# Performance work log

Measured on AMD Instinct MI355X. Metric: run time of the kernel, lower is better.

Reference implementation:

```python
import jax, jax.numpy as jnp
from jax import lax
import numpy as np

WS = 32          # window size
NUM_AA = 21      # one-hot alphabet size (hardcoded in original forward)
L = 2048         # sequence length
WIDTH = 2048
IN_SIZE = WS * NUM_AA + WS  # 704


def setup_inputs() -> dict:
    key = jax.random.key(0)
    ks = jax.random.split(key, 8)
    x = jax.random.randint(ks[0], (L,), 0, NUM_AA, dtype=jnp.int32)
    gain = np.sqrt(2.0)  # relu gain, xavier_normal init
    def xavier(k, fan_out, fan_in):
        std = gain * np.sqrt(2.0 / (fan_in + fan_out))
        return jax.random.normal(k, (fan_out, fan_in), dtype=jnp.float32) * std
    inp = {"x": x}
    dims = [(WIDTH, IN_SIZE), (WIDTH, WIDTH), (WIDTH, WIDTH), (WIDTH, WIDTH), (WIDTH, WIDTH), (1, WIDTH)]
    for i, (fo, fi) in enumerate(dims):
        inp[f"W{i}"] = xavier(ks[i + 1], fo, fi)
        inp[f"b{i}"] = jnp.zeros((fo,), dtype=jnp.float32)
    return inp


def reference(x, W0, b0, W1, b1, W2, b2, W3, b3, W4, b4, W5, b5):
    Ws = (W0, W1, W2, W3, W4, W5)
    bs = (b0, b1, b2, b3, b4, b5)
    n = x.shape[0]
    # one-hot features; the sliding window of the last WS one-hots is
    onehot = jax.nn.one_hot(x, NUM_AA, dtype=jnp.float32)          # [n, 21]
    padded = jnp.concatenate([jnp.zeros((WS - 1, NUM_AA), jnp.float32), onehot], axis=0)
    idx = jnp.arange(n)[:, None] + jnp.arange(WS)[None, :]          # [n, WS]
    xfeat = padded[idx].reshape(n, WS * NUM_AA)                     # [n, 672]

    def step(y_window, xf):
        # y_window: last WS predictions (init zeros, matching original)
        h = jnp.concatenate([xf, y_window])                         # [704]
        for W, b in zip(Ws, bs):
            h = jax.nn.relu(W @ h + b)  # relu after EVERY layer incl. output
        y_window = jnp.concatenate([y_window[1:], h])               # h: [1]
        return y_window, h[0]

    _, ys = lax.scan(step, jnp.zeros((WS,), jnp.float32), xfeat)
    return ys  # [n] predictions, equivalent of torch.cat(y_pred[ws:])
```

## Files before the change

kernel.cpp:

```cpp
#include <hip/hip_runtime.h>
#include <stdint.h>


typedef uint32_t u32;
typedef _Float16 half_t;
typedef _Float16 half2_t __attribute__((ext_vector_type(2)));

#define L_SEQ 2048
#define WIDTH 2048
#define WS    32
#define NAA   21
#define INS   704

__device__ __forceinline__ float h2f(u32 b){
  union { unsigned short u; half_t h; } c; c.u = (unsigned short)(b & 0xffffu);
  return (float)c.h;
}
__device__ __forceinline__ u32 f2h(float f){
  union { unsigned short u; half_t h; } c; c.h = (half_t)f;
  return (u32)c.u;
}
__device__ __forceinline__ float fdot2f(u32 a, u32 b, float c){
#if __has_builtin(__builtin_amdgcn_fdot2)
  union { u32 u; half2_t v; } ca, cb; ca.u = a; cb.u = b;
  return __builtin_amdgcn_fdot2(ca.v, cb.v, c, false);
#else
  return c + h2f(a)*h2f(b) + h2f(a>>16)*h2f(b>>16);
#endif
}
__device__ __forceinline__ u32 aload(u32* p){
  return __hip_atomic_load(p, __ATOMIC_RELAXED, __HIP_MEMORY_SCOPE_AGENT);
}
__device__ __forceinline__ void astore(u32* p, u32 v){
  __hip_atomic_store(p, v, __ATOMIC_RELAXED, __HIP_MEMORY_SCOPE_AGENT);
}

__global__ void k_wt(const float* __restrict__ W0, float* __restrict__ W0T){
  int tid = blockIdx.x*256 + threadIdx.x;
  if (tid < INS*WIDTH){
    int c = tid >> 11, i = tid & 2047;
    W0T[(size_t)c*WIDTH + i] = W0[(size_t)i*INS + c];
  }
}

__global__ void k_wc(const float* __restrict__ A, const float* __restrict__ B,
                     const float* __restrict__ C, const float* __restrict__ D,
                     uint4* __restrict__ Wp){
  int b = blockIdx.x; int l = b >> 11; int r = b & 2047; int j = threadIdx.x;
  const float* S = (l==0)?A:(l==1)?B:(l==2)?C:D;
  const float* rowp = S + (size_t)r*WIDTH;
  u32 o[4];
  #pragma unroll
  for (int q=0;q<4;++q){
    float a = rowp[(size_t)(2*q+0)*256 + j];
    float c2= rowp[(size_t)(2*q+1)*256 + j];
    o[q] = f2h(a) | (f2h(c2) << 16);
  }
  Wp[(size_t)b*256 + j] = make_uint4(o[0],o[1],o[2],o[3]);
}

__global__ void k_c0(const int* __restrict__ x, const float* __restrict__ W0T,
                     const float* __restrict__ b0, uint4* __restrict__ c0p){
  int t = blockIdx.x, j = threadIdx.x;
  __shared__ int cidx[WS];
  if (j < WS){
    int s = t - (WS-1) + j;
    cidx[j] = (s >= 0) ? (NAA*j + x[s]) : -1;
  }
  __syncthreads();
  float acc[8];
  #pragma unroll
  for (int k=0;k<8;++k) acc[k] = b0[256*k + j];
  for (int m=0;m<WS;++m){
    int c = cidx[m];
    if (c >= 0){
      const float* col = W0T + (size_t)c*WIDTH;
      #pragma unroll
      for (int k=0;k<8;++k) acc[k] += col[256*k + j];
    }
  }
  u32 o[4];
  #pragma unroll
  for (int q=0;q<4;++q) o[q] = f2h(acc[2*q]) | (f2h(acc[2*q+1]) << 16);
  c0p[(size_t)t*256 + j] = make_uint4(o[0],o[1],o[2],o[3]);
}

__global__ void k_reset(u32* __restrict__ hb, u32* __restrict__ pb){
  int tid = blockIdx.x*256 + threadIdx.x;
  if (tid < 3*WIDTH) hb[tid] = 0xFFFFFFFFu;
  if (tid < 256)     pb[tid] = 0xFFFFFFFFu;
}

__global__ __launch_bounds__(256, 1) void k_main(
    const float* __restrict__ W0,
    const float* __restrict__ b1, const float* __restrict__ b2,
    const float* __restrict__ b3, const float* __restrict__ b4,
    const float* __restrict__ W5, const float* __restrict__ b5p,
    const uint4* __restrict__ Wp, const uint4* __restrict__ c0p,
    u32* __restrict__ hb, u32* __restrict__ pb, float* __restrict__ out)
{
  const int j  = threadIdx.x;
  const int X  = blockIdx.x;
  const int r8 = j & 7;
  const int row = 8*X + r8;

  __shared__ float red[4][8];
  __shared__ float redp[4];

  u32 w0y[8][16];
  float w31[8];
  #pragma unroll
  for (int k=0;k<8;++k){
    const float4* bp = (const float4*)(W0 + (size_t)(256*k + j)*INS + (INS - WS));
    float arr[32];
    #pragma unroll
    for (int q=0;q<8;++q){
      float4 v = bp[q];
      arr[4*q+0]=v.x; arr[4*q+1]=v.y; arr[4*q+2]=v.z; arr[4*q+3]=v.w;
    }
    #pragma unroll
    for (int p=0;p<16;++p) w0y[k][p] = f2h(arr[2*p]) | (f2h(arr[2*p+1]) << 16);
    w31[k] = arr[31];
  }
  const float w5v = W5[row];
  const float b5v = b5p[0];
  float bsc[4] = { b1[row], b2[row], b3[row], b4[row] };

  u32 yqp[16];
  #pragma unroll
  for (int p=0;p<16;++p) yqp[p] = 0u;
  float u_part[8];
  #pragma unroll
  for (int k=0;k<8;++k) u_part[k] = 0.f;

  uint4 wrow[8];
  u32 hh[4];
  const size_t LSTR = (size_t)WIDTH*256;

  auto dolayer = [&](){
    float accv[8];
    #pragma unroll
    for (int r=0;r<8;++r){
      float a = 0.f;
      a = fdot2f(wrow[r].x, hh[0], a);
      a = fdot2f(wrow[r].y, hh[1], a);
      a = fdot2f(wrow[r].z, hh[2], a);
      a = fdot2f(wrow[r].w, hh[3], a);
      #pragma unroll
      for (int d=1; d<64; d<<=1) a += __shfl_xor(a, d);
      accv[r] = a;
    }
    if ((j & 63) == 0){
      const int w = j >> 6;
      #pragma unroll
      for (int r=0;r<8;++r) red[w][r] = accv[r];
    }
    __syncthreads();
  };

  auto pollh = [&](int l, u32 tag){
    u32 v[8];
    for(;;){
      bool ok = true;
      #pragma unroll
      for (int k=0;k<8;++k){
        v[k] = aload(&hb[l*WIDTH + 256*k + j]);
        ok &= ((v[k] >> 16) == tag);
      }
      if (ok) break;
    }
    #pragma unroll
    for (int q=0;q<4;++q) hh[q] = (v[2*q] & 0xffffu) | (v[2*q+1] << 16);
  };

  #pragma unroll 1
  for (int t=0; t<L_SEQ; ++t){
    #pragma unroll
    for (int r=0;r<8;++r) wrow[r] = Wp[(size_t)(8*X + r)*256 + j];
    uint4 c0v = c0p[(size_t)t*256 + j];

    float yprev = 0.f;
    if (t > 0){
      u32 pv;
      do { pv = aload(&pb[j]); } while ((pv >> 16) != (u32)(t-1));
      float p = h2f(pv);
      #pragma unroll
      for (int d=1; d<64; d<<=1) p += __shfl_xor(p, d);
      if ((j & 63) == 0) redp[j >> 6] = p;
      __syncthreads();
      float y = fmaxf(redp[0]+redp[1]+redp[2]+redp[3] + b5v, 0.f);
      if (X == 0 && j == 0) out[t-1] = y;
      yprev = y;
      yqp[15] |= (f2h(y) << 16);
    }

    {
      u32 c0h[4] = { c0v.x, c0v.y, c0v.z, c0v.w };
      float h0v[8];
      #pragma unroll
      for (int k=0;k<8;++k){
        u32 cb = (k & 1) ? (c0h[k>>1] >> 16) : c0h[k>>1];
        h0v[k] = fmaxf(h2f(cb) + u_part[k] + w31[k]*yprev, 0.f);
      }
      #pragma unroll
      for (int q=0;q<4;++q) hh[q] = f2h(h0v[2*q]) | (f2h(h0v[2*q+1]) << 16);
    }

    dolayer();
    if (j < 8){
      float s = fmaxf(red[0][j]+red[1][j]+red[2][j]+red[3][j] + bsc[0], 0.f);
      astore(&hb[0*WIDTH + row], ((u32)t << 16) | f2h(s));
    }
    __syncthreads();
    #pragma unroll
    for (int r=0;r<8;++r) wrow[r] = Wp[LSTR + (size_t)(8*X + r)*256 + j];
    {
      #pragma unroll
      for (int p=0;p<15;++p) yqp[p] = (yqp[p] >> 16) | (yqp[p+1] << 16);
      yqp[15] = (yqp[15] >> 16);
      #pragma unroll
      for (int k=0;k<8;++k){
        float a = 0.f;
        #pragma unroll
        for (int p=0;p<16;++p) a = fdot2f(w0y[k][p], yqp[p], a);
        u_part[k] = a;
      }
    }
    pollh(0, (u32)t);

    dolayer();
    if (j < 8){
      float s = fmaxf(red[0][j]+red[1][j]+red[2][j]+red[3][j] + bsc[1], 0.f);
      astore(&hb[1*WIDTH + row], ((u32)t << 16) | f2h(s));
    }
    __syncthreads();
    #pragma unroll
    for (int r=0;r<8;++r) wrow[r] = Wp[2*LSTR + (size_t)(8*X + r)*256 + j];
    pollh(1, (u32)t);

    dolayer();
    if (j < 8){
      float s = fmaxf(red[0][j]+red[1][j]+red[2][j]+red[3][j] + bsc[2], 0.f);
      astore(&hb[2*WIDTH + row], ((u32)t << 16) | f2h(s));
    }
    __syncthreads();
    #pragma unroll
    for (int r=0;r<8;++r) wrow[r] = Wp[3*LSTR + (size_t)(8*X + r)*256 + j];
    pollh(2, (u32)t);

    dolayer();
    if (j < 8){
      float s = fmaxf(red[0][j]+red[1][j]+red[2][j]+red[3][j] + bsc[3], 0.f);
      float pp = s * w5v;
      pp += __shfl_xor(pp, 1);
      pp += __shfl_xor(pp, 2);
      pp += __shfl_xor(pp, 4);
      if (j == 0) astore(&pb[X], ((u32)t << 16) | f2h(pp));
    }
  }

  if (X == 0){
    u32 pv;
    do { pv = aload(&pb[j]); } while ((pv >> 16) != (u32)(L_SEQ-1));
    float p = h2f(pv);
    #pragma unroll
    for (int d=1; d<64; d<<=1) p += __shfl_xor(p, d);
    if ((j & 63) == 0) redp[j >> 6] = p;
    __syncthreads();
    if (j == 0) out[L_SEQ-1] = fmaxf(redp[0]+redp[1]+redp[2]+redp[3] + b5v, 0.f);
  }
}

extern "C" void kernel_launch(void* const* d_in, const int* in_sizes, int n_in,
                              void* d_out, int out_size, void* d_ws, size_t ws_size,
                              hipStream_t stream) {
  (void)in_sizes; (void)n_in; (void)out_size; (void)ws_size;
  const int*   x  = (const int*)  d_in[0];
  const float* W0 = (const float*)d_in[1];
  const float* b0 = (const float*)d_in[2];
  const float* W1 = (const float*)d_in[3];
  const float* b1 = (const float*)d_in[4];
  const float* W2 = (const float*)d_in[5];
  const float* b2 = (const float*)d_in[6];
  const float* W3 = (const float*)d_in[7];
  const float* b3 = (const float*)d_in[8];
  const float* W4 = (const float*)d_in[9];
  const float* b4 = (const float*)d_in[10];
  const float* W5 = (const float*)d_in[11];
  const float* b5 = (const float*)d_in[12];
  float* out = (float*)d_out;
  char*  ws  = (char*)d_ws;

  constexpr size_t OFF_WP  = 0;
  constexpr size_t OFF_C0  = 33554432;
  constexpr size_t OFF_W0T = 41943040;
  constexpr size_t OFF_HB  = 47710208;
  constexpr size_t OFF_PB  = 47734784;

  uint4* Wp  = (uint4*)(ws + OFF_WP);
  uint4* c0p = (uint4*)(ws + OFF_C0);
  float* W0T = (float*)(ws + OFF_W0T);
  u32*   hb  = (u32*)  (ws + OFF_HB);
  u32*   pb  = (u32*)  (ws + OFF_PB);

  k_wt   <<<5632, 256, 0, stream>>>(W0, W0T);
  k_wc   <<<8192, 256, 0, stream>>>(W1, W2, W3, W4, Wp);
  k_c0   <<<2048, 256, 0, stream>>>(x, W0T, b0, c0p);
  k_reset<<<24,   256, 0, stream>>>(hb, pb);
  k_main <<<256,  256, 0, stream>>>(W0, b1, b2, b3, b4, W5, b5,
                                    Wp, c0p, hb, pb, out);
}
```

Measured before the change: 22.36 ms.

## Halve persistent blocks, pack hidden-state exchange into 64-bit tagged records

The persistent recurrent kernel now runs on 128 blocks with 16 rows each instead of 256 blocks with 8 rows, which halves the number of participants in each cross-block flag exchange. Hidden activations are exchanged as 64-bit records holding four fp16 values plus a tag, so each thread polls four words instead of eight. Features are now laid out contiguously per thread, so the preprocessing kernels can use vectorized float4 loads. The butterfly reduction is also restructured to pair rows across lanes, and the output partial sums are read as packed pairs by a single wavefront. In exchange, each block does twice the dot-product work per layer and holds more weight registers, which raises per-step compute latency.

```diff
diff --git a/kernel.cpp b/kernel.cpp
--- a/kernel.cpp
+++ b/kernel.cpp
@@ -3,6 +3,7 @@
 
 
 typedef uint32_t u32;
+typedef unsigned long long ull;
 typedef _Float16 half_t;
 typedef _Float16 half2_t __attribute__((ext_vector_type(2)));
 
@@ -11,6 +12,9 @@
 #define WS    32
 #define NAA   21
 #define INS   704
+#define NB    128
+#define RPB   16
+#define RECS  1024
 
 __device__ __forceinline__ float h2f(u32 b){
   union { unsigned short u; half_t h; } c; c.u = (unsigned short)(b & 0xffffu);
@@ -34,6 +38,12 @@
 __device__ __forceinline__ void astore(u32* p, u32 v){
   __hip_atomic_store(p, v, __ATOMIC_RELAXED, __HIP_MEMORY_SCOPE_AGENT);
 }
+__device__ __forceinline__ ull aload64(ull* p){
+  return __hip_atomic_load(p, __ATOMIC_RELAXED, __HIP_MEMORY_SCOPE_AGENT);
+}
+__device__ __forceinline__ void astore64(ull* p, ull v){
+  __hip_atomic_store(p, v, __ATOMIC_RELAXED, __HIP_MEMORY_SCOPE_AGENT);
+}
 
 __global__ void k_wt(const float* __restrict__ W0, float* __restrict__ W0T){
   int tid = blockIdx.x*256 + threadIdx.x;
@@ -48,15 +58,13 @@
                      uint4* __restrict__ Wp){
   int b = blockIdx.x; int l = b >> 11; int r = b & 2047; int j = threadIdx.x;
   const float* S = (l==0)?A:(l==1)?B:(l==2)?C:D;
-  const float* rowp = S + (size_t)r*WIDTH;
-  u32 o[4];
-  #pragma unroll
-  for (int q=0;q<4;++q){
-    float a = rowp[(size_t)(2*q+0)*256 + j];
-    float c2= rowp[(size_t)(2*q+1)*256 + j];
-    o[q] = f2h(a) | (f2h(c2) << 16);
-  }
-  Wp[(size_t)b*256 + j] = make_uint4(o[0],o[1],o[2],o[3]);
+  const float4* rowp = (const float4*)(S + (size_t)r*WIDTH + 8*j);
+  float4 v0 = rowp[0], v1 = rowp[1];
+  u32 o0 = f2h(v0.x) | (f2h(v0.y) << 16);
+  u32 o1 = f2h(v0.z) | (f2h(v0.w) << 16);
+  u32 o2 = f2h(v1.x) | (f2h(v1.y) << 16);
+  u32 o3 = f2h(v1.z) | (f2h(v1.w) << 16);
+  Wp[(size_t)b*256 + j] = make_uint4(o0,o1,o2,o3);
 }
 
 __global__ void k_c0(const int* __restrict__ x, const float* __restrict__ W0T,
@@ -69,14 +77,17 @@
   }
   __syncthreads();
   float acc[8];
-  #pragma unroll
-  for (int k=0;k<8;++k) acc[k] = b0[256*k + j];
+  const float4* bp = (const float4*)(b0 + 8*j);
+  float4 b00 = bp[0], b01 = bp[1];
+  acc[0]=b00.x; acc[1]=b00.y; acc[2]=b00.z; acc[3]=b00.w;
+  acc[4]=b01.x; acc[5]=b01.y; acc[6]=b01.z; acc[7]=b01.w;
   for (int m=0;m<WS;++m){
     int c = cidx[m];
     if (c >= 0){
-      const float* col = W0T + (size_t)c*WIDTH;
-      #pragma unroll
-      for (int k=0;k<8;++k) acc[k] += col[256*k + j];
+      const float4* col = (const float4*)(W0T + (size_t)c*WIDTH + 8*j);
+      float4 u0 = col[0], u1 = col[1];
+      acc[0]+=u0.x; acc[1]+=u0.y; acc[2]+=u0.z; acc[3]+=u0.w;
+      acc[4]+=u1.x; acc[5]+=u1.y; acc[6]+=u1.z; acc[7]+=u1.w;
     }
   }
   u32 o[4];
@@ -88,7 +99,7 @@
 __global__ void k_reset(u32* __restrict__ hb, u32* __restrict__ pb){
   int tid = blockIdx.x*256 + threadIdx.x;
   if (tid < 3*WIDTH) hb[tid] = 0xFFFFFFFFu;
-  if (tid < 256)     pb[tid] = 0xFFFFFFFFu;
+  if (tid < NB)      pb[tid] = 0xFFFFFFFFu;
 }
 
 __global__ __launch_bounds__(256, 1) void k_main(
@@ -97,21 +108,20 @@
     const float* __restrict__ b3, const float* __restrict__ b4,
     const float* __restrict__ W5, const float* __restrict__ b5p,
     const uint4* __restrict__ Wp, const uint4* __restrict__ c0p,
-    u32* __restrict__ hb, u32* __restrict__ pb, float* __restrict__ out)
+    ull* hbq, ull* pbq, u32* pb, float* __restrict__ out)
 {
-  const int j  = threadIdx.x;
-  const int X  = blockIdx.x;
-  const int r8 = j & 7;
-  const int row = 8*X + r8;
-
-  __shared__ float red[4][8];
-  __shared__ float redp[4];
+  const int j = threadIdx.x;
+  const int X = blockIdx.x;
+  const int row16 = RPB*X + (j & 15);
+
+  __shared__ float red[4][RPB];
+  __shared__ float ylds;
 
   u32 w0y[8][16];
   float w31[8];
   #pragma unroll
-  for (int k=0;k<8;++k){
-    const float4* bp = (const float4*)(W0 + (size_t)(256*k + j)*INS + (INS - WS));
+  for (int e=0;e<8;++e){
+    const float4* bp = (const float4*)(W0 + (size_t)(8*j + e)*INS + (INS - WS));
     float arr[32];
     #pragma unroll
     for (int q=0;q<8;++q){
@@ -119,155 +129,174 @@
       arr[4*q+0]=v.x; arr[4*q+1]=v.y; arr[4*q+2]=v.z; arr[4*q+3]=v.w;
     }
     #pragma unroll
-    for (int p=0;p<16;++p) w0y[k][p] = f2h(arr[2*p]) | (f2h(arr[2*p+1]) << 16);
-    w31[k] = arr[31];
-  }
-  const float w5v = W5[row];
+    for (int p=0;p<16;++p) w0y[e][p] = f2h(arr[2*p]) | (f2h(arr[2*p+1]) << 16);
+    w31[e] = arr[31];
+  }
+  const float w5v = W5[row16];
   const float b5v = b5p[0];
-  float bsc[4] = { b1[row], b2[row], b3[row], b4[row] };
+  float bsc[4] = { b1[row16], b2[row16], b3[row16], b4[row16] };
 
   u32 yqp[16];
   #pragma unroll
   for (int p=0;p<16;++p) yqp[p] = 0u;
   float u_part[8];
   #pragma unroll
-  for (int k=0;k<8;++k) u_part[k] = 0.f;
-
-  uint4 wrow[8];
+  for (int e=0;e<8;++e) u_part[e] = 0.f;
+
+  uint4 wrow[RPB];
   u32 hh[4];
-  const size_t LSTR = (size_t)WIDTH*256;
-
-  auto dolayer = [&](){
-    float accv[8];
-    #pragma unroll
-    for (int r=0;r<8;++r){
+  const int w = j >> 6;
+
+  auto prefetch = [&](int lw){
+    #pragma unroll
+    for (int r=0;r<RPB;++r)
+      wrow[r] = Wp[((size_t)lw*2048 + RPB*X + r)*256 + j];
+  };
+
+  auto doreduce = [&](){
+    float accv[RPB];
+    #pragma unroll
+    for (int r=0;r<RPB;++r){
       float a = 0.f;
       a = fdot2f(wrow[r].x, hh[0], a);
       a = fdot2f(wrow[r].y, hh[1], a);
       a = fdot2f(wrow[r].z, hh[2], a);
       a = fdot2f(wrow[r].w, hh[3], a);
-      #pragma unroll
-      for (int d=1; d<64; d<<=1) a += __shfl_xor(a, d);
       accv[r] = a;
     }
-    if ((j & 63) == 0){
-      const int w = j >> 6;
-      #pragma unroll
-      for (int r=0;r<8;++r) red[w][r] = accv[r];
+    #pragma unroll
+    for (int r=0;r<RPB;r+=2){
+      float a = accv[r]   + __shfl_xor(accv[r],   1);
+      float b = accv[r+1] + __shfl_xor(accv[r+1], 1);
+      float m = (j & 1) ? b : a;
+      m += __shfl_xor(m, 2);
+      m += __shfl_xor(m, 4);
+      m += __shfl_xor(m, 8);
+      m += __shfl_xor(m, 16);
+      m += __shfl_xor(m, 32);
+      if ((j & 63) < 2) red[w][r + (j & 1)] = m;
     }
     __syncthreads();
   };
 
+  auto emit_h = [&](int l, u32 tag, float bias){
+    float s = 0.f;
+    if (j < 16) s = fmaxf(red[0][j]+red[1][j]+red[2][j]+red[3][j] + bias, 0.f);
+    if (j < 64){
+      u32 hs = f2h(s);
+      u32 lo = __shfl(hs, 2*j);
+      u32 hi = __shfl(hs, 2*j + 1);
+      if (j < 8)
+        astore64(hbq + (size_t)l*RECS + 8*X + j,
+                 ((ull)tag << 32) | (ull)(lo | (hi << 16)));
+    }
+  };
+
   auto pollh = [&](int l, u32 tag){
-    u32 v[8];
+    ull* base = hbq + (size_t)l*RECS + 4*j;
+    ull r0,r1,r2,r3;
     for(;;){
-      bool ok = true;
-      #pragma unroll
-      for (int k=0;k<8;++k){
-        v[k] = aload(&hb[l*WIDTH + 256*k + j]);
-        ok &= ((v[k] >> 16) == tag);
-      }
-      if (ok) break;
-    }
-    #pragma unroll
-    for (int q=0;q<4;++q) hh[q] = (v[2*q] & 0xffffu) | (v[2*q+1] << 16);
+      r0 = aload64(base+0); r1 = aload64(base+1);
+      r2 = aload64(base+2); r3 = aload64(base+3);
+      if (((u32)(r0>>32)==tag) & ((u32)(r1>>32)==tag) &
+          ((u32)(r2>>32)==tag) & ((u32)(r3>>32)==tag)) break;
+    }
+    hh[0]=(u32)r0; hh[1]=(u32)r1; hh[2]=(u32)r2; hh[3]=(u32)r3;
   };
 
   #pragma unroll 1
   for (int t=0; t<L_SEQ; ++t){
-    #pragma unroll
-    for (int r=0;r<8;++r) wrow[r] = Wp[(size_t)(8*X + r)*256 + j];
+    prefetch(0);
     uint4 c0v = c0p[(size_t)t*256 + j];
 
-    float yprev = 0.f;
     if (t > 0){
-      u32 pv;
-      do { pv = aload(&pb[j]); } while ((pv >> 16) != (u32)(t-1));
-      float p = h2f(pv);
-      #pragma unroll
-      for (int d=1; d<64; d<<=1) p += __shfl_xor(p, d);
-      if ((j & 63) == 0) redp[j >> 6] = p;
-      __syncthreads();
-      float y = fmaxf(redp[0]+redp[1]+redp[2]+redp[3] + b5v, 0.f);
-      if (X == 0 && j == 0) out[t-1] = y;
-      yprev = y;
-      yqp[15] |= (f2h(y) << 16);
-    }
+      if (j < 64){
+        u32 lo, hi; ull v;
+        const u32 tprev = (u32)(t-1);
+        for(;;){
+          v = aload64(pbq + j);
+          lo = (u32)v; hi = (u32)(v >> 32);
+          if (((lo>>16)==tprev) & ((hi>>16)==tprev)) break;
+        }
+        float p = h2f(lo) + h2f(hi);
+        #pragma unroll
+        for (int d=1; d<64; d<<=1) p += __shfl_xor(p, d);
+        if (j == 0){
+          float y = fmaxf(p + b5v, 0.f);
+          ylds = y;
+          if (X == 0) out[t-1] = y;
+        }
+      }
+    } else {
+      if (j == 0) ylds = 0.f;
+    }
+    __syncthreads();
+    float yprev = ylds;
+    if (t > 0) yqp[15] |= (f2h(yprev) << 16);
 
     {
       u32 c0h[4] = { c0v.x, c0v.y, c0v.z, c0v.w };
       float h0v[8];
       #pragma unroll
-      for (int k=0;k<8;++k){
-        u32 cb = (k & 1) ? (c0h[k>>1] >> 16) : c0h[k>>1];
-        h0v[k] = fmaxf(h2f(cb) + u_part[k] + w31[k]*yprev, 0.f);
+      for (int e=0;e<8;++e){
+        u32 cb = (e & 1) ? (c0h[e>>1] >> 16) : c0h[e>>1];
+        h0v[e] = fmaxf(h2f(cb) + u_part[e] + w31[e]*yprev, 0.f);
       }
       #pragma unroll
       for (int q=0;q<4;++q) hh[q] = f2h(h0v[2*q]) | (f2h(h0v[2*q+1]) << 16);
     }
 
-    dolayer();
-    if (j < 8){
-      float s = fmaxf(red[0][j]+red[1][j]+red[2][j]+red[3][j] + bsc[0], 0.f);
-      astore(&hb[0*WIDTH + row], ((u32)t << 16) | f2h(s));
-    }
-    __syncthreads();
-    #pragma unroll
-    for (int r=0;r<8;++r) wrow[r] = Wp[LSTR + (size_t)(8*X + r)*256 + j];
+    doreduce();
+    emit_h(0, (u32)t, bsc[0]);
+    prefetch(1);
     {
       #pragma unroll
       for (int p=0;p<15;++p) yqp[p] = (yqp[p] >> 16) | (yqp[p+1] << 16);
       yqp[15] = (yqp[15] >> 16);
       #pragma unroll
-      for (int k=0;k<8;++k){
+      for (int e=0;e<8;++e){
         float a = 0.f;
         #pragma unroll
-        for (int p=0;p<16;++p) a = fdot2f(w0y[k][p], yqp[p], a);
-        u_part[k] = a;
+        for (int p=0;p<16;++p) a = fdot2f(w0y[e][p], yqp[p], a);
+        u_part[e] = a;
       }
     }
     pollh(0, (u32)t);
 
-    dolayer();
-    if (j < 8){
-      float s = fmaxf(red[0][j]+red[1][j]+red[2][j]+red[3][j] + bsc[1], 0.f);
-      astore(&hb[1*WIDTH + row], ((u32)t << 16) | f2h(s));
-    }
-    __syncthreads();
-    #pragma unroll
-    for (int r=0;r<8;++r) wrow[r] = Wp[2*LSTR + (size_t)(8*X + r)*256 + j];
+    doreduce();
+    emit_h(1, (u32)t, bsc[1]);
+    prefetch(2);
     pollh(1, (u32)t);
 
-    dolayer();
-    if (j < 8){
-      float s = fmaxf(red[0][j]+red[1][j]+red[2][j]+red[3][j] + bsc[2], 0.f);
-      astore(&hb[2*WIDTH + row], ((u32)t << 16) | f2h(s));
-    }
-    __syncthreads();
-    #pragma unroll
-    for (int r=0;r<8;++r) wrow[r] = Wp[3*LSTR + (size_t)(8*X + r)*256 + j];
+    doreduce();
+    emit_h(2, (u32)t, bsc[2]);
+    prefetch(3);
     pollh(2, (u32)t);
 
-    dolayer();
-    if (j < 8){
+    doreduce();
+    if (j < 16){
       float s = fmaxf(red[0][j]+red[1][j]+red[2][j]+red[3][j] + bsc[3], 0.f);
       float pp = s * w5v;
       pp += __shfl_xor(pp, 1);
       pp += __shfl_xor(pp, 2);
       pp += __shfl_xor(pp, 4);
+      pp += __shfl_xor(pp, 8);
       if (j == 0) astore(&pb[X], ((u32)t << 16) | f2h(pp));
     }
   }
 
-  if (X == 0){
-    u32 pv;
-    do { pv = aload(&pb[j]); } while ((pv >> 16) != (u32)(L_SEQ-1));
-    float p = h2f(pv);
+  if (X == 0 && j < 64){
+    u32 lo, hi; ull v;
+    const u32 tl = (u32)(L_SEQ-1);
+    for(;;){
+      v = aload64(pbq + j);
+      lo = (u32)v; hi = (u32)(v >> 32);
+      if (((lo>>16)==tl) & ((hi>>16)==tl)) break;
+    }
+    float p = h2f(lo) + h2f(hi);
     #pragma unroll
     for (int d=1; d<64; d<<=1) p += __shfl_xor(p, d);
-    if ((j & 63) == 0) redp[j >> 6] = p;
-    __syncthreads();
-    if (j == 0) out[L_SEQ-1] = fmaxf(redp[0]+redp[1]+redp[2]+redp[3] + b5v, 0.f);
+    if (j == 0) out[L_SEQ-1] = fmaxf(p + b5v, 0.f);
   }
 }
 
@@ -301,12 +330,14 @@
   uint4* c0p = (uint4*)(ws + OFF_C0);
   float* W0T = (float*)(ws + OFF_W0T);
   u32*   hb  = (u32*)  (ws + OFF_HB);
+  ull*   hbq = (ull*)  (ws + OFF_HB);
   u32*   pb  = (u32*)  (ws + OFF_PB);
+  ull*   pbq = (ull*)  (ws + OFF_PB);
 
   k_wt   <<<5632, 256, 0, stream>>>(W0, W0T);
   k_wc   <<<8192, 256, 0, stream>>>(W1, W2, W3, W4, Wp);
   k_c0   <<<2048, 256, 0, stream>>>(x, W0T, b0, c0p);
   k_reset<<<24,   256, 0, stream>>>(hb, pb);
-  k_main <<<256,  256, 0, stream>>>(W0, b1, b2, b3, b4, W5, b5,
-                                    Wp, c0p, hb, pb, out);
-}
+  k_main <<<NB,   256, 0, stream>>>(W0, b1, b2, b3, b4, W5, b5,
+                                    Wp, c0p, hbq, pbq, pb, out);
+}
```

After: 31.45 ms. +40.7%, slower.

## Keep layer weights in registers and pack hidden-state flags into 64-bit records

Applied to the files above, without the earlier changes.

All four hidden layers' fp16 weight slices are now loaded into registers once, instead of being re-fetched from global memory every timestep. Hidden activations are exchanged as 64-bit records holding a tag and four fp16 values, so each poll needs four loads per thread instead of eight. The per-layer reduction pairs rows to halve the shuffle count, and the LDS buffers are double-buffered so one __syncthreads per layer can go. Column ordering is changed to a contiguous float2 layout throughout, and polling is software-pipelined. The cost is much higher register pressure and a more intricate packing scheme.

```diff
diff --git a/kernel.cpp b/kernel.cpp
--- a/kernel.cpp
+++ b/kernel.cpp
@@ -3,6 +3,7 @@
 
 
 typedef uint32_t u32;
+typedef unsigned long long ull;
 typedef _Float16 half_t;
 typedef _Float16 half2_t __attribute__((ext_vector_type(2)));
 
@@ -11,6 +12,8 @@
 #define WS    32
 #define NAA   21
 #define INS   704
+#define NB    256
+#define RECS  1024
 
 __device__ __forceinline__ float h2f(u32 b){
   union { unsigned short u; half_t h; } c; c.u = (unsigned short)(b & 0xffffu);
@@ -34,6 +37,12 @@
 __device__ __forceinline__ void astore(u32* p, u32 v){
   __hip_atomic_store(p, v, __ATOMIC_RELAXED, __HIP_MEMORY_SCOPE_AGENT);
 }
+__device__ __forceinline__ ull aload64(ull* p){
+  return __hip_atomic_load(p, __ATOMIC_RELAXED, __HIP_MEMORY_SCOPE_AGENT);
+}
+__device__ __forceinline__ void astore64(ull* p, ull v){
+  __hip_atomic_store(p, v, __ATOMIC_RELAXED, __HIP_MEMORY_SCOPE_AGENT);
+}
 
 __global__ void k_wt(const float* __restrict__ W0, float* __restrict__ W0T){
   int tid = blockIdx.x*256 + threadIdx.x;
@@ -48,13 +57,12 @@
                      uint4* __restrict__ Wp){
   int b = blockIdx.x; int l = b >> 11; int r = b & 2047; int j = threadIdx.x;
   const float* S = (l==0)?A:(l==1)?B:(l==2)?C:D;
-  const float* rowp = S + (size_t)r*WIDTH;
+  const float2* p2 = (const float2*)(S + (size_t)r*WIDTH);
   u32 o[4];
   #pragma unroll
-  for (int q=0;q<4;++q){
-    float a = rowp[(size_t)(2*q+0)*256 + j];
-    float c2= rowp[(size_t)(2*q+1)*256 + j];
-    o[q] = f2h(a) | (f2h(c2) << 16);
+  for (int k=0;k<4;++k){
+    float2 v = p2[256*k + j];
+    o[k] = f2h(v.x) | (f2h(v.y) << 16);
   }
   Wp[(size_t)b*256 + j] = make_uint4(o[0],o[1],o[2],o[3]);
 }
@@ -68,27 +76,28 @@
     cidx[j] = (s >= 0) ? (NAA*j + x[s]) : -1;
   }
   __syncthreads();
-  float acc[8];
-  #pragma unroll
-  for (int k=0;k<8;++k) acc[k] = b0[256*k + j];
+  float ax[4], ay[4];
+  const float2* b2p = (const float2*)b0;
+  #pragma unroll
+  for (int k=0;k<4;++k){ float2 v = b2p[256*k + j]; ax[k]=v.x; ay[k]=v.y; }
   for (int m=0;m<WS;++m){
     int c = cidx[m];
     if (c >= 0){
-      const float* col = W0T + (size_t)c*WIDTH;
-      #pragma unroll
-      for (int k=0;k<8;++k) acc[k] += col[256*k + j];
+      const float2* w2 = (const float2*)(W0T + (size_t)c*WIDTH);
+      #pragma unroll
+      for (int k=0;k<4;++k){ float2 v = w2[256*k + j]; ax[k]+=v.x; ay[k]+=v.y; }
     }
   }
   u32 o[4];
   #pragma unroll
-  for (int q=0;q<4;++q) o[q] = f2h(acc[2*q]) | (f2h(acc[2*q+1]) << 16);
+  for (int k=0;k<4;++k) o[k] = f2h(ax[k]) | (f2h(ay[k]) << 16);
   c0p[(size_t)t*256 + j] = make_uint4(o[0],o[1],o[2],o[3]);
 }
 
 __global__ void k_reset(u32* __restrict__ hb, u32* __restrict__ pb){
   int tid = blockIdx.x*256 + threadIdx.x;
   if (tid < 3*WIDTH) hb[tid] = 0xFFFFFFFFu;
-  if (tid < 256)     pb[tid] = 0xFFFFFFFFu;
+  if (tid < NB)      pb[tid] = 0xFFFFFFFFu;
 }
 
 __global__ __launch_bounds__(256, 1) void k_main(
@@ -97,31 +106,42 @@
     const float* __restrict__ b3, const float* __restrict__ b4,
     const float* __restrict__ W5, const float* __restrict__ b5p,
     const uint4* __restrict__ Wp, const uint4* __restrict__ c0p,
-    u32* __restrict__ hb, u32* __restrict__ pb, float* __restrict__ out)
+    ull* hbq, u32* pb, float* __restrict__ out)
 {
   const int j  = threadIdx.x;
   const int X  = blockIdx.x;
   const int r8 = j & 7;
   const int row = 8*X + r8;
 
-  __shared__ float red[4][8];
+  __shared__ float red[2][4][8];
   __shared__ float redp[4];
+
+  uint4 wreg[4][8];
+  #pragma unroll
+  for (int l=0;l<4;++l)
+    #pragma unroll
+    for (int r=0;r<8;++r)
+      wreg[l][r] = Wp[((size_t)l*2048 + 8*X + r)*256 + j];
 
   u32 w0y[8][16];
   float w31[8];
   #pragma unroll
-  for (int k=0;k<8;++k){
-    const float4* bp = (const float4*)(W0 + (size_t)(256*k + j)*INS + (INS - WS));
-    float arr[32];
-    #pragma unroll
-    for (int q=0;q<8;++q){
-      float4 v = bp[q];
-      arr[4*q+0]=v.x; arr[4*q+1]=v.y; arr[4*q+2]=v.z; arr[4*q+3]=v.w;
-    }
-    #pragma unroll
-    for (int p=0;p<16;++p) w0y[k][p] = f2h(arr[2*p]) | (f2h(arr[2*p+1]) << 16);
-    w31[k] = arr[31];
-  }
+  for (int k=0;k<4;++k)
+    #pragma unroll
+    for (int s=0;s<2;++s){
+      int e = 2*k+s;
+      int rr = 512*k + 2*j + s;
+      const float4* bp = (const float4*)(W0 + (size_t)rr*INS + (INS - WS));
+      float arr[32];
+      #pragma unroll
+      for (int q=0;q<8;++q){
+        float4 v = bp[q];
+        arr[4*q+0]=v.x; arr[4*q+1]=v.y; arr[4*q+2]=v.z; arr[4*q+3]=v.w;
+      }
+      #pragma unroll
+      for (int p=0;p<16;++p) w0y[e][p] = f2h(arr[2*p]) | (f2h(arr[2*p+1]) << 16);
+      w31[e] = arr[31];
+    }
   const float w5v = W5[row];
   const float b5v = b5p[0];
   float bsc[4] = { b1[row], b2[row], b3[row], b4[row] };
@@ -131,62 +151,86 @@
   for (int p=0;p<16;++p) yqp[p] = 0u;
   float u_part[8];
   #pragma unroll
-  for (int k=0;k<8;++k) u_part[k] = 0.f;
-
-  uint4 wrow[8];
+  for (int e=0;e<8;++e) u_part[e] = 0.f;
+
   u32 hh[4];
-  const size_t LSTR = (size_t)WIDTH*256;
-
-  auto dolayer = [&](){
+  const int w = j >> 6;
+
+  auto doreduce = [&](const uint4 (&wr)[8], int buf){
     float accv[8];
     #pragma unroll
     for (int r=0;r<8;++r){
       float a = 0.f;
-      a = fdot2f(wrow[r].x, hh[0], a);
-      a = fdot2f(wrow[r].y, hh[1], a);
-      a = fdot2f(wrow[r].z, hh[2], a);
-      a = fdot2f(wrow[r].w, hh[3], a);
-      #pragma unroll
-      for (int d=1; d<64; d<<=1) a += __shfl_xor(a, d);
+      a = fdot2f(wr[r].x, hh[0], a);
+      a = fdot2f(wr[r].y, hh[1], a);
+      a = fdot2f(wr[r].z, hh[2], a);
+      a = fdot2f(wr[r].w, hh[3], a);
       accv[r] = a;
     }
-    if ((j & 63) == 0){
-      const int w = j >> 6;
-      #pragma unroll
-      for (int r=0;r<8;++r) red[w][r] = accv[r];
+    #pragma unroll
+    for (int r=0;r<8;r+=2){
+      float a = accv[r]   + __shfl_xor(accv[r],   1);
+      float b = accv[r+1] + __shfl_xor(accv[r+1], 1);
+      float m = (j & 1) ? b : a;
+      m += __shfl_xor(m, 2);
+      m += __shfl_xor(m, 4);
+      m += __shfl_xor(m, 8);
+      m += __shfl_xor(m, 16);
+      m += __shfl_xor(m, 32);
+      if ((j & 63) < 2) red[buf][w][r + (j & 1)] = m;
     }
     __syncthreads();
   };
 
+  auto emit_h = [&](int l, u32 tag, float bias, int buf){
+    float s = 0.f;
+    if (j < 8)
+      s = fmaxf(red[buf][0][j]+red[buf][1][j]+red[buf][2][j]+red[buf][3][j] + bias, 0.f);
+    if (j < 64){
+      u32 hs = f2h(s);
+      u32 lo = __shfl(hs, 2*(j & 3));
+      u32 hi = __shfl(hs, 2*(j & 3) + 1);
+      if (j < 4)
+        astore64(hbq + (size_t)l*RECS + (X>>6)*256 + 4*(X&63) + j,
+                 ((ull)tag << 32) | (ull)(lo | (hi << 16)));
+    }
+  };
+
   auto pollh = [&](int l, u32 tag){
-    u32 v[8];
+    ull* base = hbq + (size_t)l*RECS;
+    ull A0,A1,A2,A3,B0,B1,B2,B3;
+    A0=aload64(base+     j); A1=aload64(base+ 256+j);
+    A2=aload64(base+ 512+j); A3=aload64(base+ 768+j);
+    B0=aload64(base+     j); B1=aload64(base+ 256+j);
+    B2=aload64(base+ 512+j); B3=aload64(base+ 768+j);
     for(;;){
-      bool ok = true;
-      #pragma unroll
-      for (int k=0;k<8;++k){
-        v[k] = aload(&hb[l*WIDTH + 256*k + j]);
-        ok &= ((v[k] >> 16) == tag);
-      }
-      if (ok) break;
-    }
-    #pragma unroll
-    for (int q=0;q<4;++q) hh[q] = (v[2*q] & 0xffffu) | (v[2*q+1] << 16);
+      if (((u32)(A0>>32)==tag) & ((u32)(A1>>32)==tag) &
+          ((u32)(A2>>32)==tag) & ((u32)(A3>>32)==tag)) break;
+      A0=B0; A1=B1; A2=B2; A3=B3;
+      B0=aload64(base+     j); B1=aload64(base+ 256+j);
+      B2=aload64(base+ 512+j); B3=aload64(base+ 768+j);
+    }
+    hh[0]=(u32)A0; hh[1]=(u32)A1; hh[2]=(u32)A2; hh[3]=(u32)A3;
   };
 
   #pragma unroll 1
   for (int t=0; t<L_SEQ; ++t){
-    #pragma unroll
-    for (int r=0;r<8;++r) wrow[r] = Wp[(size_t)(8*X + r)*256 + j];
     uint4 c0v = c0p[(size_t)t*256 + j];
 
     float yprev = 0.f;
     if (t > 0){
-      u32 pv;
-      do { pv = aload(&pb[j]); } while ((pv >> 16) != (u32)(t-1));
-      float p = h2f(pv);
+      const u32 tprev = (u32)(t-1);
+      u32 A = aload(&pb[j]);
+      u32 B = aload(&pb[j]);
+      for(;;){
+        if ((A >> 16) == tprev) break;
+        A = B;
+        B = aload(&pb[j]);
+      }
+      float p = h2f(A);
       #pragma unroll
       for (int d=1; d<64; d<<=1) p += __shfl_xor(p, d);
-      if ((j & 63) == 0) redp[j >> 6] = p;
+      if ((j & 63) == 0) redp[w] = p;
       __syncthreads();
       float y = fmaxf(redp[0]+redp[1]+redp[2]+redp[3] + b5v, 0.f);
       if (X == 0 && j == 0) out[t-1] = y;
@@ -196,76 +240,64 @@
 
     {
       u32 c0h[4] = { c0v.x, c0v.y, c0v.z, c0v.w };
-      float h0v[8];
-      #pragma unroll
-      for (int k=0;k<8;++k){
-        u32 cb = (k & 1) ? (c0h[k>>1] >> 16) : c0h[k>>1];
-        h0v[k] = fmaxf(h2f(cb) + u_part[k] + w31[k]*yprev, 0.f);
-      }
-      #pragma unroll
-      for (int q=0;q<4;++q) hh[q] = f2h(h0v[2*q]) | (f2h(h0v[2*q+1]) << 16);
-    }
-
-    dolayer();
-    if (j < 8){
-      float s = fmaxf(red[0][j]+red[1][j]+red[2][j]+red[3][j] + bsc[0], 0.f);
-      astore(&hb[0*WIDTH + row], ((u32)t << 16) | f2h(s));
-    }
-    __syncthreads();
-    #pragma unroll
-    for (int r=0;r<8;++r) wrow[r] = Wp[LSTR + (size_t)(8*X + r)*256 + j];
+      #pragma unroll
+      for (int k=0;k<4;++k){
+        float h0a = fmaxf(h2f(c0h[k])       + u_part[2*k]   + w31[2*k]*yprev,   0.f);
+        float h0b = fmaxf(h2f(c0h[k] >> 16) + u_part[2*k+1] + w31[2*k+1]*yprev, 0.f);
+        hh[k] = f2h(h0a) | (f2h(h0b) << 16);
+      }
+    }
+
+    doreduce(wreg[0], 0);
+    emit_h(0, (u32)t, bsc[0], 0);
     {
       #pragma unroll
       for (int p=0;p<15;++p) yqp[p] = (yqp[p] >> 16) | (yqp[p+1] << 16);
       yqp[15] = (yqp[15] >> 16);
       #pragma unroll
-      for (int k=0;k<8;++k){
+      for (int e=0;e<8;++e){
         float a = 0.f;
         #pragma unroll
-        for (int p=0;p<16;++p) a = fdot2f(w0y[k][p], yqp[p], a);
-        u_part[k] = a;
+        for (int p=0;p<16;++p) a = fdot2f(w0y[e][p], yqp[p], a);
+        u_part[e] = a;
       }
     }
     pollh(0, (u32)t);
 
-    dolayer();
-    if (j < 8){
-      float s = fmaxf(red[0][j]+red[1][j]+red[2][j]+red[3][j] + bsc[1], 0.f);
-      astore(&hb[1*WIDTH + row], ((u32)t << 16) | f2h(s));
-    }
-    __syncthreads();
-    #pragma unroll
-    for (int r=0;r<8;++r) wrow[r] = Wp[2*LSTR + (size_t)(8*X + r)*256 + j];
+    doreduce(wreg[1], 1);
+    emit_h(1, (u32)t, bsc[1], 1);
     pollh(1, (u32)t);
 
-    dolayer();
-    if (j < 8){
-      float s = fmaxf(red[0][j]+red[1][j]+red[2][j]+red[3][j] + bsc[2], 0.f);
-      astore(&hb[2*WIDTH + row], ((u32)t << 16) | f2h(s));
-    }
-    __syncthreads();
-    #pragma unroll
-    for (int r=0;r<8;++r) wrow[r] = Wp[3*LSTR + (size_t)(8*X + r)*256 + j];
+    doreduce(wreg[2], 0);
+    emit_h(2, (u32)t, bsc[2], 0);
     pollh(2, (u32)t);
 
-    dolayer();
-    if (j < 8){
-      float s = fmaxf(red[0][j]+red[1][j]+red[2][j]+red[3][j] + bsc[3], 0.f);
-      float pp = s * w5v;
-      pp += __shfl_xor(pp, 1);
-      pp += __shfl_xor(pp, 2);
-      pp += __shfl_xor(pp, 4);
-      if (j == 0) astore(&pb[X], ((u32)t << 16) | f2h(pp));
+    doreduce(wreg[3], 1);
+    {
+      float s = 0.f;
+      if (j < 8)
+        s = fmaxf(red[1][0][j]+red[1][1][j]+red[1][2][j]+red[1][3][j] + bsc[3], 0.f);
+      if (j < 64){
+        float pp = s * w5v;
+        pp += __shfl_xor(pp, 1);
+        pp += __shfl_xor(pp, 2);
+        pp += __shfl_xor(pp, 4);
+        if (j == 0) astore(&pb[X], ((u32)t << 16) | f2h(pp));
+      }
     }
   }
 
   if (X == 0){
-    u32 pv;
-    do { pv = aload(&pb[j]); } while ((pv >> 16) != (u32)(L_SEQ-1));
-    float p = h2f(pv);
+    const u32 tl = (u32)(L_SEQ-1);
+    u32 A = aload(&pb[j]);
+    for(;;){
+      if ((A >> 16) == tl) break;
+      A = aload(&pb[j]);
+    }
+    float p = h2f(A);
     #pragma unroll
     for (int d=1; d<64; d<<=1) p += __shfl_xor(p, d);
-    if ((j & 63) == 0) redp[j >> 6] = p;
+    if ((j & 63) == 0) redp[w] = p;
     __syncthreads();
     if (j == 0) out[L_SEQ-1] = fmaxf(redp[0]+redp[1]+redp[2]+redp[3] + b5v, 0.f);
   }
@@ -301,12 +333,13 @@
   uint4* c0p = (uint4*)(ws + OFF_C0);
   float* W0T = (float*)(ws + OFF_W0T);
   u32*   hb  = (u32*)  (ws + OFF_HB);
+  ull*   hbq = (ull*)  (ws + OFF_HB);
   u32*   pb  = (u32*)  (ws + OFF_PB);
 
   k_wt   <<<5632, 256, 0, stream>>>(W0, W0T);
   k_wc   <<<8192, 256, 0, stream>>>(W1, W2, W3, W4, Wp);
   k_c0   <<<2048, 256, 0, stream>>>(x, W0T, b0, c0p);
   k_reset<<<24,   256, 0, stream>>>(hb, pb);
-  k_main <<<256,  256, 0, stream>>>(W0, b1, b2, b3, b4, W5, b5,
-                                    Wp, c0p, hb, pb, out);
-}
+  k_main <<<NB,   256, 0, stream>>>(W0, b1, b2, b3, b4, W5, b5,
+                                    Wp, c0p, hbq, pb, out);
+}
```

Result: slower. 29.72 ms (+32.9%).

## Pipeline layers across block groups with register-resident weights

Applied to the files above, without the earlier changes.

The persistent kernel is split into four groups of 64 blocks, one per hidden layer. Each block keeps its 32 rows of fp16 weights in registers for the whole sequence instead of reloading 8 rows per layer per step, and each group polls only the previous layer's output buffer. The output layer's dot product moves into group 0, which reads layer-4 activations directly, and the y-window weights for W0 are stored in a workspace buffer instead of registers. Sleep-based backoff is added to the polling loops. This removes per-step weight reloads and lets different layers overlap, at the cost of higher register pressure, a multi-stage shuffle reduction, and added latency from the sleep calls.

```diff
diff --git a/kernel.cpp b/kernel.cpp
--- a/kernel.cpp
+++ b/kernel.cpp
@@ -11,6 +11,11 @@
 #define WS    32
 #define NAA   21
 #define INS   704
+#define NB    256
+#define GSZ   64
+#define SLP_FAIL 2
+#define SLP_IDLE 20
+#define N_IDLE   3
 
 __device__ __forceinline__ float h2f(u32 b){
   union { unsigned short u; half_t h; } c; c.u = (unsigned short)(b & 0xffffu);
@@ -48,14 +53,11 @@
                      uint4* __restrict__ Wp){
   int b = blockIdx.x; int l = b >> 11; int r = b & 2047; int j = threadIdx.x;
   const float* S = (l==0)?A:(l==1)?B:(l==2)?C:D;
-  const float* rowp = S + (size_t)r*WIDTH;
+  const float* row = S + (size_t)r*WIDTH;
   u32 o[4];
   #pragma unroll
-  for (int q=0;q<4;++q){
-    float a = rowp[(size_t)(2*q+0)*256 + j];
-    float c2= rowp[(size_t)(2*q+1)*256 + j];
-    o[q] = f2h(a) | (f2h(c2) << 16);
-  }
+  for (int q=0;q<4;++q)
+    o[q] = f2h(row[256*(2*q)+j]) | (f2h(row[256*(2*q+1)+j]) << 16);
   Wp[(size_t)b*256 + j] = make_uint4(o[0],o[1],o[2],o[3]);
 }
 
@@ -85,10 +87,17 @@
   c0p[(size_t)t*256 + j] = make_uint4(o[0],o[1],o[2],o[3]);
 }
 
-__global__ void k_reset(u32* __restrict__ hb, u32* __restrict__ pb){
+__global__ void k_wy(const float* __restrict__ W0, u32* __restrict__ wyb){
+  int b = blockIdx.x; int k = b >> 4, p = b & 15; int j = threadIdx.x;
+  int col = 256*k + j;
+  float a = W0[(size_t)col*INS + (INS-WS) + 2*p];
+  float c = W0[(size_t)col*INS + (INS-WS) + 2*p + 1];
+  wyb[(size_t)b*256 + j] = f2h(a) | (f2h(c) << 16);
+}
+
+__global__ void k_reset(u32* __restrict__ hb){
   int tid = blockIdx.x*256 + threadIdx.x;
-  if (tid < 3*WIDTH) hb[tid] = 0xFFFFFFFFu;
-  if (tid < 256)     pb[tid] = 0xFFFFFFFFu;
+  if (tid < 4*WIDTH) hb[tid] = 0xFFFFFFFFu;
 }
 
 __global__ __launch_bounds__(256, 1) void k_main(
@@ -97,177 +106,201 @@
     const float* __restrict__ b3, const float* __restrict__ b4,
     const float* __restrict__ W5, const float* __restrict__ b5p,
     const uint4* __restrict__ Wp, const uint4* __restrict__ c0p,
-    u32* __restrict__ hb, u32* __restrict__ pb, float* __restrict__ out)
+    const u32* __restrict__ wyb,
+    u32* hb, float* __restrict__ out)
 {
   const int j  = threadIdx.x;
   const int X  = blockIdx.x;
-  const int r8 = j & 7;
-  const int row = 8*X + r8;
-
-  __shared__ float red[4][8];
+  const int g  = X >> 6;
+  const int Xl = X & 63;
+  const int lw = j & 63;
+  const int w  = j >> 6;
+
+  __shared__ float red[4][32];
   __shared__ float redp[4];
 
-  u32 w0y[8][16];
-  float w31[8];
+  uint4 wreg[32];
   #pragma unroll
-  for (int k=0;k<8;++k){
-    const float4* bp = (const float4*)(W0 + (size_t)(256*k + j)*INS + (INS - WS));
-    float arr[32];
-    #pragma unroll
-    for (int q=0;q<8;++q){
-      float4 v = bp[q];
-      arr[4*q+0]=v.x; arr[4*q+1]=v.y; arr[4*q+2]=v.z; arr[4*q+3]=v.w;
-    }
-    #pragma unroll
-    for (int p=0;p<16;++p) w0y[k][p] = f2h(arr[2*p]) | (f2h(arr[2*p+1]) << 16);
-    w31[k] = arr[31];
-  }
-  const float w5v = W5[row];
-  const float b5v = b5p[0];
-  float bsc[4] = { b1[row], b2[row], b3[row], b4[row] };
-
-  u32 yqp[16];
-  #pragma unroll
-  for (int p=0;p<16;++p) yqp[p] = 0u;
-  float u_part[8];
-  #pragma unroll
-  for (int k=0;k<8;++k) u_part[k] = 0.f;
-
-  uint4 wrow[8];
+  for (int r=0;r<32;++r)
+    wreg[r] = Wp[((size_t)g*2048 + 32*Xl + r)*256 + j];
+
+  const float* bp = (g==0)?b1:(g==1)?b2:(g==2)?b3:b4;
+  float bv = 0.f;
+  if (j < 32) bv = bp[32*Xl + j];
+
   u32 hh[4];
-  const size_t LSTR = (size_t)WIDTH*256;
-
-  auto dolayer = [&](){
-    float accv[8];
-    #pragma unroll
-    for (int r=0;r<8;++r){
+
+  auto doreduce_emit = [&](u32 tag){
+    float c32[32];
+    #pragma unroll
+    for (int r=0;r<32;++r){
       float a = 0.f;
-      a = fdot2f(wrow[r].x, hh[0], a);
-      a = fdot2f(wrow[r].y, hh[1], a);
-      a = fdot2f(wrow[r].z, hh[2], a);
-      a = fdot2f(wrow[r].w, hh[3], a);
-      #pragma unroll
-      for (int d=1; d<64; d<<=1) a += __shfl_xor(a, d);
-      accv[r] = a;
-    }
-    if ((j & 63) == 0){
-      const int w = j >> 6;
-      #pragma unroll
-      for (int r=0;r<8;++r) red[w][r] = accv[r];
+      a = fdot2f(wreg[r].x, hh[0], a);
+      a = fdot2f(wreg[r].y, hh[1], a);
+      a = fdot2f(wreg[r].z, hh[2], a);
+      a = fdot2f(wreg[r].w, hh[3], a);
+      c32[r] = a;
+    }
+    float c16[16];
+    #pragma unroll
+    for (int i=0;i<16;++i){
+      float v = c32[2*i]   + __shfl_xor(c32[2*i],   1);
+      float u = c32[2*i+1] + __shfl_xor(c32[2*i+1], 1);
+      c16[i] = (lw & 1) ? u : v;
+    }
+    float c8[8];
+    #pragma unroll
+    for (int i=0;i<8;++i){
+      float v = c16[2*i]   + __shfl_xor(c16[2*i],   2);
+      float u = c16[2*i+1] + __shfl_xor(c16[2*i+1], 2);
+      c8[i] = (lw & 2) ? u : v;
+    }
+    float c4[4];
+    #pragma unroll
+    for (int i=0;i<4;++i){
+      float v = c8[2*i]   + __shfl_xor(c8[2*i],   4);
+      float u = c8[2*i+1] + __shfl_xor(c8[2*i+1], 4);
+      c4[i] = (lw & 4) ? u : v;
+    }
+    float c2[2];
+    #pragma unroll
+    for (int i=0;i<2;++i){
+      float v = c4[2*i]   + __shfl_xor(c4[2*i],   8);
+      float u = c4[2*i+1] + __shfl_xor(c4[2*i+1], 8);
+      c2[i] = (lw & 8) ? u : v;
+    }
+    float v1 = c2[0] + __shfl_xor(c2[0], 16);
+    float u1 = c2[1] + __shfl_xor(c2[1], 16);
+    float c1 = (lw & 16) ? u1 : v1;
+    float tot = c1 + __shfl_xor(c1, 32);
+    if (lw < 32) red[w][lw] = tot;
+    __syncthreads();
+    if (j < 32){
+      float s = fmaxf(red[0][j]+red[1][j]+red[2][j]+red[3][j] + bv, 0.f);
+      astore(&hb[(size_t)g*WIDTH + 32*Xl + j], (tag << 16) | f2h(s));
     }
     __syncthreads();
   };
 
-  auto pollh = [&](int l, u32 tag){
-    u32 v[8];
+  auto pollh = [&](int gin, u32 tag){
+    u32 rec[8];
+    u32* base = hb + (size_t)gin*WIDTH;
     for(;;){
+      #pragma unroll
+      for (int k=0;k<8;++k) rec[k] = aload(base + 256*k + j);
       bool ok = true;
       #pragma unroll
-      for (int k=0;k<8;++k){
-        v[k] = aload(&hb[l*WIDTH + 256*k + j]);
-        ok &= ((v[k] >> 16) == tag);
+      for (int k=0;k<8;++k) ok &= ((rec[k] >> 16) == tag);
+      if (ok) break;
+      __builtin_amdgcn_s_sleep(SLP_FAIL);
+    }
+    #pragma unroll
+    for (int q=0;q<4;++q) hh[q] = (rec[2*q] & 0xffffu) | (rec[2*q+1] << 16);
+  };
+
+  for (int i=0;i<g;++i) __builtin_amdgcn_s_sleep(SLP_IDLE);
+
+  if (g > 0){
+    const int gin = g - 1;
+    #pragma unroll 1
+    for (int t=0; t<L_SEQ; ++t){
+      pollh(gin, (u32)t);
+      doreduce_emit((u32)t);
+      for (int i=0;i<N_IDLE;++i) __builtin_amdgcn_s_sleep(SLP_IDLE);
+    }
+  } else {
+    float w5f[8], w31v[8];
+    #pragma unroll
+    for (int k=0;k<8;++k){
+      w5f[k]  = W5[256*k + j];
+      w31v[k] = W0[(size_t)(256*k + j)*INS + (INS-1)];
+    }
+    const float b5v = b5p[0];
+    u32 yqp[16];
+    #pragma unroll
+    for (int p=0;p<16;++p) yqp[p] = 0u;
+    float u_part[8];
+    #pragma unroll
+    for (int k=0;k<8;++k) u_part[k] = 0.f;
+
+    #pragma unroll 1
+    for (int t=0; t<L_SEQ; ++t){
+      float y = 0.f;
+      if (t > 0){
+        u32 rec[8];
+        u32* base = hb + (size_t)3*WIDTH;
+        const u32 tag = (u32)(t-1);
+        for(;;){
+          #pragma unroll
+          for (int k=0;k<8;++k) rec[k] = aload(base + 256*k + j);
+          bool ok = true;
+          #pragma unroll
+          for (int k=0;k<8;++k) ok &= ((rec[k] >> 16) == tag);
+          if (ok) break;
+          __builtin_amdgcn_s_sleep(SLP_FAIL);
+        }
+        float yp = 0.f;
+        #pragma unroll
+        for (int k=0;k<8;++k) yp += w5f[k] * h2f(rec[k]);
+        #pragma unroll
+        for (int d=1; d<64; d<<=1) yp += __shfl_xor(yp, d);
+        if (lw == 0) redp[w] = yp;
+        __syncthreads();
+        y = fmaxf(redp[0]+redp[1]+redp[2]+redp[3] + b5v, 0.f);
+        if (X == 0 && j == 0) out[t-1] = y;
+        yqp[15] |= (f2h(y) << 16);
       }
-      if (ok) break;
-    }
-    #pragma unroll
-    for (int q=0;q<4;++q) hh[q] = (v[2*q] & 0xffffu) | (v[2*q+1] << 16);
-  };
-
-  #pragma unroll 1
-  for (int t=0; t<L_SEQ; ++t){
-    #pragma unroll
-    for (int r=0;r<8;++r) wrow[r] = Wp[(size_t)(8*X + r)*256 + j];
-    uint4 c0v = c0p[(size_t)t*256 + j];
-
-    float yprev = 0.f;
-    if (t > 0){
-      u32 pv;
-      do { pv = aload(&pb[j]); } while ((pv >> 16) != (u32)(t-1));
-      float p = h2f(pv);
-      #pragma unroll
-      for (int d=1; d<64; d<<=1) p += __shfl_xor(p, d);
-      if ((j & 63) == 0) redp[j >> 6] = p;
+      uint4 c0v = c0p[(size_t)t*256 + j];
+      {
+        u32 c0h[4] = { c0v.x, c0v.y, c0v.z, c0v.w };
+        float h0v[8];
+        #pragma unroll
+        for (int q=0;q<4;++q){
+          h0v[2*q]   = fmaxf(h2f(c0h[q])       + u_part[2*q]   + w31v[2*q]*y,   0.f);
+          h0v[2*q+1] = fmaxf(h2f(c0h[q] >> 16) + u_part[2*q+1] + w31v[2*q+1]*y, 0.f);
+        }
+        #pragma unroll
+        for (int q=0;q<4;++q) hh[q] = f2h(h0v[2*q]) | (f2h(h0v[2*q+1]) << 16);
+      }
+      doreduce_emit((u32)t);
+      {
+        #pragma unroll
+        for (int p=0;p<15;++p) yqp[p] = (yqp[p] >> 16) | (yqp[p+1] << 16);
+        yqp[15] = (yqp[15] >> 16);
+        #pragma unroll
+        for (int k=0;k<8;++k){
+          float a = 0.f;
+          #pragma unroll
+          for (int p=0;p<16;++p)
+            a = fdot2f(wyb[(size_t)(16*k+p)*256 + j], yqp[p], a);
+          u_part[k] = a;
+        }
+      }
+      for (int i=0;i<N_IDLE;++i) __builtin_amdgcn_s_sleep(SLP_IDLE);
+    }
+
+    if (X == 0){
+      u32 rec[8];
+      u32* base = hb + (size_t)3*WIDTH;
+      const u32 tag = (u32)(L_SEQ-1);
+      for(;;){
+        #pragma unroll
+        for (int k=0;k<8;++k) rec[k] = aload(base + 256*k + j);
+        bool ok = true;
+        #pragma unroll
+        for (int k=0;k<8;++k) ok &= ((rec[k] >> 16) == tag);
+        if (ok) break;
+        __builtin_amdgcn_s_sleep(SLP_FAIL);
+      }
+      float yp = 0.f;
+      #pragma unroll
+      for (int k=0;k<8;++k) yp += w5f[k] * h2f(rec[k]);
+      #pragma unroll
+      for (int d=1; d<64; d<<=1) yp += __shfl_xor(yp, d);
+      if (lw == 0) redp[w] = yp;
       __syncthreads();
-      float y = fmaxf(redp[0]+redp[1]+redp[2]+redp[3] + b5v, 0.f);
-      if (X == 0 && j == 0) out[t-1] = y;
-      yprev = y;
-      yqp[15] |= (f2h(y) << 16);
-    }
-
-    {
-      u32 c0h[4] = { c0v.x, c0v.y, c0v.z, c0v.w };
-      float h0v[8];
-      #pragma unroll
-      for (int k=0;k<8;++k){
-        u32 cb = (k & 1) ? (c0h[k>>1] >> 16) : c0h[k>>1];
-        h0v[k] = fmaxf(h2f(cb) + u_part[k] + w31[k]*yprev, 0.f);
-      }
-      #pragma unroll
-      for (int q=0;q<4;++q) hh[q] = f2h(h0v[2*q]) | (f2h(h0v[2*q+1]) << 16);
-    }
-
-    dolayer();
-    if (j < 8){
-      float s = fmaxf(red[0][j]+red[1][j]+red[2][j]+red[3][j] + bsc[0], 0.f);
-      astore(&hb[0*WIDTH + row], ((u32)t << 16) | f2h(s));
-    }
-    __syncthreads();
-    #pragma unroll
-    for (int r=0;r<8;++r) wrow[r] = Wp[LSTR + (size_t)(8*X + r)*256 + j];
-    {
-      #pragma unroll
-      for (int p=0;p<15;++p) yqp[p] = (yqp[p] >> 16) | (yqp[p+1] << 16);
-      yqp[15] = (yqp[15] >> 16);
-      #pragma unroll
-      for (int k=0;k<8;++k){
-        float a = 0.f;
-        #pragma unroll
-        for (int p=0;p<16;++p) a = fdot2f(w0y[k][p], yqp[p], a);
-        u_part[k] = a;
-      }
-    }
-    pollh(0, (u32)t);
-
-    dolayer();
-    if (j < 8){
-      float s = fmaxf(red[0][j]+red[1][j]+red[2][j]+red[3][j] + bsc[1], 0.f);
-      astore(&hb[1*WIDTH + row], ((u32)t << 16) | f2h(s));
-    }
-    __syncthreads();
-    #pragma unroll
-    for (int r=0;r<8;++r) wrow[r] = Wp[2*LSTR + (size_t)(8*X + r)*256 + j];
-    pollh(1, (u32)t);
-
-    dolayer();
-    if (j < 8){
-      float s = fmaxf(red[0][j]+red[1][j]+red[2][j]+red[3][j] + bsc[2], 0.f);
-      astore(&hb[2*WIDTH + row], ((u32)t << 16) | f2h(s));
-    }
-    __syncthreads();
-    #pragma unroll
-    for (int r=0;r<8;++r) wrow[r] = Wp[3*LSTR + (size_t)(8*X + r)*256 + j];
-    pollh(2, (u32)t);
-
-    dolayer();
-    if (j < 8){
-      float s = fmaxf(red[0][j]+red[1][j]+red[2][j]+red[3][j] + bsc[3], 0.f);
-      float pp = s * w5v;
-      pp += __shfl_xor(pp, 1);
-      pp += __shfl_xor(pp, 2);
-      pp += __shfl_xor(pp, 4);
-      if (j == 0) astore(&pb[X], ((u32)t << 16) | f2h(pp));
-    }
-  }
-
-  if (X == 0){
-    u32 pv;
-    do { pv = aload(&pb[j]); } while ((pv >> 16) != (u32)(L_SEQ-1));
-    float p = h2f(pv);
-    #pragma unroll
-    for (int d=1; d<64; d<<=1) p += __shfl_xor(p, d);
-    if ((j & 63) == 0) redp[j >> 6] = p;
-    __syncthreads();
-    if (j == 0) out[L_SEQ-1] = fmaxf(redp[0]+redp[1]+redp[2]+redp[3] + b5v, 0.f);
+      if (j == 0) out[L_SEQ-1] = fmaxf(redp[0]+redp[1]+redp[2]+redp[3] + b5v, 0.f);
+    }
   }
 }
 
@@ -294,19 +327,20 @@
   constexpr size_t OFF_WP  = 0;
   constexpr size_t OFF_C0  = 33554432;
   constexpr size_t OFF_W0T = 41943040;
-  constexpr size_t OFF_HB  = 47710208;
-  constexpr size_t OFF_PB  = 47734784;
+  constexpr size_t OFF_WY  = 47710208;
+  constexpr size_t OFF_HB  = 47841280;
 
   uint4* Wp  = (uint4*)(ws + OFF_WP);
   uint4* c0p = (uint4*)(ws + OFF_C0);
   float* W0T = (float*)(ws + OFF_W0T);
+  u32*   wyb = (u32*)  (ws + OFF_WY);
   u32*   hb  = (u32*)  (ws + OFF_HB);
-  u32*   pb  = (u32*)  (ws + OFF_PB);
 
   k_wt   <<<5632, 256, 0, stream>>>(W0, W0T);
   k_wc   <<<8192, 256, 0, stream>>>(W1, W2, W3, W4, Wp);
   k_c0   <<<2048, 256, 0, stream>>>(x, W0T, b0, c0p);
-  k_reset<<<24,   256, 0, stream>>>(hb, pb);
-  k_main <<<256,  256, 0, stream>>>(W0, b1, b2, b3, b4, W5, b5,
-                                    Wp, c0p, hb, pb, out);
-}
+  k_wy   <<<128,  256, 0, stream>>>(W0, wyb);
+  k_reset<<<32,   256, 0, stream>>>(hb);
+  k_main <<<NB,   256, 0, stream>>>(W0, b1, b2, b3, b4, W5, b5,
+                                    Wp, c0p, wyb, hb, out);
+}
```

New measurement: 20.08 ms. -10.2%, faster.
